# Kernel optimization log

Measured on AMD Instinct MI355X. Metric: run time of the kernel, lower is better.

## Reference

```python
import jax, jax.numpy as jnp
import numpy as np

K_MIN = 30.0
TAU = 1e-06
BETA = 0.9
LAMBDA_MAX = 0.1
LAMBDA_SCALE = 1.0

N, D_OUT, N_MODULES, N_CONTEXTS = 262144, 128, 64, 16


def setup_inputs() -> dict:
    key = jax.random.key(0)
    k1, k2, k3, k4 = jax.random.split(key, 4)
    Y_hat = jax.random.normal(k1, (N, D_OUT), dtype=jnp.float32)
    context_weights = jax.random.uniform(k2, (N, N_CONTEXTS), dtype=jnp.float32)
    M_pinv = jax.random.normal(k3, (N_MODULES, D_OUT), dtype=jnp.float32) * 0.1
    C_prior = jax.random.normal(k4, (N_CONTEXTS, N_MODULES, N_MODULES), dtype=jnp.float32) * 0.1
    # Buffers exactly as registered in __init__
    ema_Sigma = jnp.broadcast_to(jnp.eye(N_MODULES, dtype=jnp.float32), (N_CONTEXTS, N_MODULES, N_MODULES))
    ema_sigma_sq = jnp.ones((N_CONTEXTS, N_MODULES), dtype=jnp.float32)
    ema_initialized = jnp.zeros((N_CONTEXTS,), dtype=bool)
    return {"Y_hat": Y_hat, "context_weights": context_weights, "M_pinv": M_pinv,
            "C_prior": C_prior, "ema_Sigma": ema_Sigma, "ema_sigma_sq": ema_sigma_sq,
            "ema_initialized": ema_initialized}


def reference(Y_hat, context_weights, M_pinv, C_prior, ema_Sigma, ema_sigma_sq, ema_initialized):
    # Z_hat: [N, m]
    Z = Y_hat @ M_pinv.T
    wsum = context_weights.sum(axis=0)            # [T] == eff_n per context
    active = wsum >= K_MIN                        # context skipping, vectorized
    # Weighted mean per context: [T, m]
    mu = (context_weights.T @ Z) / wsum[:, None]
    # Weighted covariance: sum_n w_norm * (z-mu)(z-mu)^T == E_w[zz^T] - mu mu^T
    w_norm = context_weights / wsum[None, :]      # [N, T]
    S = jnp.einsum('nt,nm,nk->tmk', w_norm, Z, Z)  # [T, m, m]
    Sigma = S - mu[:, :, None] * mu[:, None, :]
    # EMA sigma_sq update (no-grad in original -> stop_gradient)
    Sigma_sg = jax.lax.stop_gradient(Sigma)
    diag_init = jnp.diagonal(Sigma_sg, axis1=1, axis2=2)                       # first-call branch
    diag_ema = jnp.diagonal(BETA * ema_Sigma + (1.0 - BETA) * Sigma_sg, axis1=1, axis2=2)
    sigma_sq = jnp.where(ema_initialized[:, None], diag_ema, diag_init)        # [T, m]
    std = jnp.sqrt(sigma_sq + TAU)
    denom = std[:, :, None] * std[:, None, :]
    C_hat = jnp.clip(Sigma / (denom + TAU), -1.0, 1.0)
    loss_t = jnp.sum((C_hat - C_prior) ** 2, axis=(1, 2)) / wsum               # [T]
    n_active = jnp.sum(active)
    total = jnp.sum(jnp.where(active, loss_t, 0.0))
    total = jnp.where(n_active > 0,
                      LAMBDA_MAX * LAMBDA_SCALE * total / jnp.maximum(n_active, 1).astype(total.dtype),
                      jnp.zeros((), total.dtype))
    return total
```

## Files before the change

### kernel.cpp

```cpp
#include <hip/hip_runtime.h>
#include <stdint.h>

#define N_ROWS 262144
#define D_OUTC 128
#define M_MOD  64
#define T_CTX  16

#define ZB_OFF   ((size_t)0)
#define ZB_BYTES ((size_t)M_MOD * N_ROWS * 2)
#define WT_OFF   (ZB_OFF + ZB_BYTES)
#define WT_BYTES ((size_t)T_CTX * N_ROWS * 2)
#define SS_OFF   (WT_OFF + WT_BYTES)
#define SS_BYTES ((size_t)T_CTX * M_MOD * M_MOD * 4)
#define B_OFF    (SS_OFF + SS_BYTES)
#define B_BYTES  ((size_t)T_CTX * M_MOD * 4)
#define WSUM_OFF (B_OFF + B_BYTES)
#define WSUM_BYTES ((size_t)64)
#define LT_OFF   (WSUM_OFF + WSUM_BYTES)
#define LT_BYTES ((size_t)64)
#define PSS_OFF  (LT_OFF + LT_BYTES)
#define PSS_BYTES ((size_t)256 * T_CTX * M_MOD * M_MOD * 2)
#define NEED_BIG (PSS_OFF + PSS_BYTES)

typedef __attribute__((ext_vector_type(4))) float f32x4;
typedef __attribute__((ext_vector_type(8))) _Float16 f16x8;
typedef __attribute__((ext_vector_type(2))) _Float16 h2;

union FR { uint4 u; f16x8 v; h2 h[4]; };

__device__ __forceinline__ float bf2f(unsigned short u) {
  return __uint_as_float(((unsigned int)u) << 16);
}
__device__ __forceinline__ unsigned short f2bf(float f) {
  unsigned int x = __float_as_uint(f);
  return (unsigned short)((x + 0x7fffu + ((x >> 16) & 1u)) >> 16);
}
__device__ __forceinline__ h2 cvt_pkrtz(float a, float b) {
  return __builtin_bit_cast(h2, __builtin_amdgcn_cvt_pkrtz(a, b));
}
#if __has_builtin(__builtin_amdgcn_fdot2)
__device__ __forceinline__ float fdot2f(h2 a, h2 b, float c) {
  return __builtin_amdgcn_fdot2(a, b, c, false);
}
#else
__device__ __forceinline__ float fdot2f(h2 a, h2 b, float c) {
  return c + (float)a[0] * (float)b[0] + (float)a[1] * (float)b[1];
}
#endif

#define WAITVM(N) asm volatile("s_waitcnt vmcnt(" #N ")" ::: "memory")
#define SBAR() do { __builtin_amdgcn_s_barrier(); __builtin_amdgcn_sched_barrier(0); } while (0)

__global__ __launch_bounds__(256) void wtr_kernel(const float* __restrict__ W,
                                                  _Float16* __restrict__ Wt)
{
  __shared__ float Wf[16][260];
  const int tid = threadIdx.x;
  const int n0  = blockIdx.x * 256;
  {
    const float4* src = (const float4*)(W + (size_t)(n0 + tid) * T_CTX);
#pragma unroll
    for (int q = 0; q < 4; ++q) {
      float4 v = src[q];
      Wf[q * 4 + 0][tid] = v.x; Wf[q * 4 + 1][tid] = v.y;
      Wf[q * 4 + 2][tid] = v.z; Wf[q * 4 + 3][tid] = v.w;
    }
  }
  __syncthreads();
  const int t = tid >> 4, c0 = (tid & 15) * 16;
  FR o[2];
#pragma unroll
  for (int j = 0; j < 2; ++j)
#pragma unroll
    for (int p = 0; p < 4; ++p)
      o[j].h[p] = cvt_pkrtz(Wf[t][c0 + j * 8 + 2 * p], Wf[t][c0 + j * 8 + 2 * p + 1]);
  uint4* dst = (uint4*)(Wt + (size_t)t * N_ROWS + n0 + c0);
  dst[0] = o[0].u; dst[1] = o[1].u;
}

__global__ __launch_bounds__(256, 6) void zk_kernel(
    const float* __restrict__ Y, const float* __restrict__ Mp,
    _Float16* __restrict__ Zbt)
{
  __shared__ __align__(16) _Float16 Mpl[64 * 128];
  const int tid = threadIdx.x;
  const int l   = tid & 63;
  const int wv  = tid >> 6;
  const int g   = l >> 4;
  const int col = l & 15;
  {
    const int m  = tid >> 2;
    const int dq = tid & 3;
#pragma unroll
    for (int i = 0; i < 4; ++i) {
      const int s = dq * 4 + i;
      const float* mp = Mp + (size_t)m * D_OUTC + s * 8;
      float4 a = *(const float4*)mp;
      float4 b = *(const float4*)(mp + 4);
      FR o;
      o.h[0] = cvt_pkrtz(a.x, a.y); o.h[1] = cvt_pkrtz(a.z, a.w);
      o.h[2] = cvt_pkrtz(b.x, b.y); o.h[3] = cvt_pkrtz(b.z, b.w);
      const int ss = (s & ~7) | ((s & 7) ^ (m & 7));
      *(uint4*)((char*)&Mpl[0] + m * 256 + ss * 16) = o.u;
    }
  }
  __syncthreads();
#pragma unroll
  for (int it = 0; it < 2; ++it) {
    const int n0 = (blockIdx.x * 2 + it) * 64;
    const int nr = n0 + wv * 16 + col;
    const float* __restrict__ yr = Y + (size_t)nr * D_OUTC;
    float4 yv[8];
#pragma unroll
    for (int ks = 0; ks < 4; ++ks) {
      yv[2 * ks]     = *(const float4*)(yr + ks * 32 + g * 8);
      yv[2 * ks + 1] = *(const float4*)(yr + ks * 32 + g * 8 + 4);
    }
    f32x4 acc[4];
#pragma unroll
    for (int qi = 0; qi < 4; ++qi) acc[qi] = (f32x4){0.f, 0.f, 0.f, 0.f};
#pragma unroll
    for (int ks = 0; ks < 4; ++ks) {
      const float* f0 = (const float*)&yv[2 * ks];
      const float* f1 = (const float*)&yv[2 * ks + 1];
      FR B;
      B.h[0] = cvt_pkrtz(f0[0], f0[1]); B.h[1] = cvt_pkrtz(f0[2], f0[3]);
      B.h[2] = cvt_pkrtz(f1[0], f1[1]); B.h[3] = cvt_pkrtz(f1[2], f1[3]);
#pragma unroll
      for (int qi = 0; qi < 4; ++qi) {
        const int m = qi * 16 + col;
        const int s = ks * 4 + g;
        FR A;
        A.u = *(const uint4*)((char*)&Mpl[0] + m * 256 + 16 * ((s & ~7) | ((s & 7) ^ (m & 7))));
        acc[qi] = __builtin_amdgcn_mfma_f32_16x16x32_f16(A.v, B.v, acc[qi], 0, 0, 0);
      }
    }
#pragma unroll
    for (int qi = 0; qi < 4; ++qi)
#pragma unroll
      for (int i = 0; i < 4; ++i)
        Zbt[(size_t)(qi * 16 + g * 4 + i) * N_ROWS + n0 + wv * 16 + col] =
            (_Float16)acc[qi][i];
  }
}

#define SS_NS 256
#define NCH   16
template <bool PARTIAL>
__global__ __launch_bounds__(512, 4) void ss_kernel(
    const _Float16* __restrict__ Zbt, const _Float16* __restrict__ Wt,
    float* __restrict__ SS, float* __restrict__ Bm,
    unsigned short* __restrict__ Pss)
{
  __shared__ __align__(16) _Float16 Zl[4][64 * 64];
  __shared__ __align__(16) _Float16 Wlds[8 * 1024];
  const int tid = threadIdx.x;
  const int l   = tid & 63;
  const int wv  = tid >> 6;
  const int g   = l >> 4;
  const int col = l & 15;
  const int ns  = blockIdx.x & (SS_NS - 1);
  const int cg  = blockIdx.x >> 8;
  const int ctx = cg * 8 + wv;
  const int n0b = ns * 1024;

  f32x4 acc[4][4];
  f32x4 accB[4];
#pragma unroll
  for (int a = 0; a < 4; ++a) {
    accB[a] = (f32x4){0.f, 0.f, 0.f, 0.f};
#pragma unroll
    for (int b = 0; b < 4; ++b) acc[a][b] = (f32x4){0.f, 0.f, 0.f, 0.f};
  }
  FR ones;
#pragma unroll
  for (int j = 0; j < 4; ++j) ones.h[j] = (h2){(_Float16)1.f, (_Float16)1.f};

#pragma unroll
  for (int k = 0; k < 2; ++k) {
    const _Float16* wsrc = Wt + (size_t)ctx * N_ROWS + n0b + k * 512 + l * 8;
    __builtin_amdgcn_global_load_lds((const unsigned int*)wsrc,
        (unsigned int*)((char*)&Wlds[0] + wv * 2048 + k * 1024), 16, 0, 0);
  }
  const int zrow  = 8 * wv + (l >> 3);
  const int zslot = l & 7;
  auto stage = [&](int c) {
    const int n0 = n0b + c * 64;
    const _Float16* src = Zbt + (size_t)zrow * N_ROWS + n0 + 8 * (zslot ^ (zrow & 7));
    __builtin_amdgcn_global_load_lds((const unsigned int*)src,
        (unsigned int*)((char*)&Zl[c & 3][0] + wv * 1024 + l * 16), 16, 0, 0);
  };

  stage(0); stage(1); stage(2);
  WAITVM(2);
  SBAR();

  for (int c = 0; c < NCH; ++c) {
    if (c + 3 < NCH) stage(c + 3);
    const char* zb = (const char*)&Zl[c & 3][0];
    const char* wb = (const char*)&Wlds[0] + wv * 2048 + c * 128;
#pragma unroll
    for (int s = 0; s < 2; ++s) {
      FR wfr;
      wfr.u = *(const uint4*)(wb + s * 64 + g * 16);
      FR fr[4];
#pragma unroll
      for (int qi = 0; qi < 4; ++qi) {
        const int r = qi * 16 + col;
        fr[qi].u = *(const uint4*)(zb + r * 128 + 16 * ((s * 4 + g) ^ (r & 7)));
      }
      __builtin_amdgcn_s_setprio(1);
#pragma unroll
      for (int qi = 0; qi < 4; ++qi) {
        FR A;
#pragma unroll
        for (int j = 0; j < 4; ++j) A.h[j] = fr[qi].h[j] * wfr.h[j];
        accB[qi] = __builtin_amdgcn_mfma_f32_16x16x32_f16(A.v, ones.v, accB[qi], 0, 0, 0);
#pragma unroll
        for (int ki = 0; ki < 4; ++ki)
          acc[qi][ki] = __builtin_amdgcn_mfma_f32_16x16x32_f16(A.v, fr[ki].v, acc[qi][ki], 0, 0, 0);
      }
      __builtin_amdgcn_s_setprio(0);
    }
    if (c + 3 < NCH)       { WAITVM(2); SBAR(); }
    else if (c == NCH - 3) { WAITVM(1); SBAR(); }
    else if (c == NCH - 2) { WAITVM(0); SBAR(); }
  }

  if (col == 0) {
#pragma unroll
    for (int qi = 0; qi < 4; ++qi)
#pragma unroll
      for (int i = 0; i < 4; ++i)
        atomicAdd(&Bm[ctx * 64 + qi * 16 + g * 4 + i], accB[qi][i]);
  }
  if (PARTIAL) {
    unsigned short* P = Pss + ((size_t)ns * 16 + ctx) * 4096;
#pragma unroll
    for (int qi = 0; qi < 4; ++qi)
#pragma unroll
      for (int ki = 0; ki < 4; ++ki)
#pragma unroll
        for (int i = 0; i < 4; ++i)
          P[(qi * 16 + g * 4 + i) * 64 + ki * 16 + col] = f2bf(acc[qi][ki][i]);
  } else {
#pragma unroll
    for (int qi = 0; qi < 4; ++qi)
#pragma unroll
      for (int ki = 0; ki < 4; ++ki)
#pragma unroll
        for (int i = 0; i < 4; ++i)
          atomicAdd(&SS[(size_t)ctx * 4096 + (qi * 16 + g * 4 + i) * 64 + ki * 16 + col],
                    acc[qi][ki][i]);
  }
}

__global__ __launch_bounds__(256) void wsk_kernel(const _Float16* __restrict__ Wt,
                                                  float* __restrict__ wsum)
{
  const int tid = threadIdx.x;
  const int t = blockIdx.x >> 2, q = blockIdx.x & 3;
  const uint4* base = (const uint4*)(Wt + (size_t)t * N_ROWS + q * 65536);
  const h2 one2 = {(_Float16)1.f, (_Float16)1.f};
  float s = 0.f;
  for (int i = tid; i < 8192; i += 256) {
    uint4 v = base[i];
    const h2* h = (const h2*)&v;
#pragma unroll
    for (int j = 0; j < 4; ++j) s = fdot2f(h[j], one2, s);
  }
  s += __shfl_xor(s, 1);  s += __shfl_xor(s, 2);
  s += __shfl_xor(s, 4);  s += __shfl_xor(s, 8);
  s += __shfl_xor(s, 16); s += __shfl_xor(s, 32);
  __shared__ float red[4];
  if ((tid & 63) == 0) red[tid >> 6] = s;
  __syncthreads();
  if (tid == 0) atomicAdd(&wsum[t], red[0] + red[1] + red[2] + red[3]);
}

__global__ __launch_bounds__(256) void ssred_kernel(
    const unsigned short* __restrict__ Pss, float* __restrict__ SS)
{
  const int e = blockIdx.x * 256 + threadIdx.x;
  float s = 0.f;
#pragma unroll 8
  for (int b = 0; b < 256; ++b)
    s += bf2f(Pss[(size_t)b * 65536 + e]);
  SS[e] = s;
}

__global__ __launch_bounds__(64) void fin1_kernel(
    const float* __restrict__ SS, const float* __restrict__ Bm,
    const float* __restrict__ wsum, const float* __restrict__ Cp,
    const float* __restrict__ emaS, const unsigned char* __restrict__ inited,
    float* __restrict__ LT)
{
  const int t = blockIdx.x, m = threadIdx.x;
  __shared__ float muL[64], stdL[64];
  const float ws  = wsum[t];
  const float inv = 1.0f / ws;
  const float mu  = Bm[t * 64 + m] * inv;
  {
    float Smm = SS[(size_t)t * 4096 + m * 65] * inv - mu * mu;
    float de  = 0.9f * emaS[(size_t)t * 4096 + m * 65] + 0.1f * Smm;
    float sq  = inited[t] ? de : Smm;
    muL[m]  = mu;
    stdL[m] = sqrtf(sq + 1e-6f);
  }
  __syncthreads();
  const float sm = stdL[m];
  const float* SSr = SS + (size_t)t * 4096 + m * 64;
  const float* Cpr = Cp + (size_t)t * 4096 + m * 64;
  float acc = 0.f;
#pragma unroll
  for (int k = 0; k < 64; ++k) {
    float Sig = SSr[k] * inv - mu * muL[k];
    float den = sm * stdL[k] + 1e-6f;
    float ch  = fminf(1.f, fmaxf(-1.f, Sig / den));
    float d   = ch - Cpr[k];
    acc = fmaf(d, d, acc);
  }
#pragma unroll
  for (int o = 1; o < 64; o <<= 1) acc += __shfl_xor(acc, o);
  if (m == 0) LT[t] = acc * inv;
}

__global__ __launch_bounds__(64) void fin2_kernel(
    const float* __restrict__ LT, const float* __restrict__ wsum,
    float* __restrict__ out)
{
  const int l = threadIdx.x;
  float lt = 0.f, act = 0.f;
  if (l < 16) {
    float ws = wsum[l];
    if (ws >= 30.0f) { act = 1.f; lt = LT[l]; }
  }
#pragma unroll
  for (int o = 1; o < 16; o <<= 1) {
    lt  += __shfl_xor(lt, o);
    act += __shfl_xor(act, o);
  }
  if (l == 0) out[0] = (act > 0.f) ? (0.1f * 1.0f * lt / act) : 0.f;
}

extern "C" void kernel_launch(void* const* d_in, const int* in_sizes, int n_in,
                              void* d_out, int out_size, void* d_ws, size_t ws_size,
                              hipStream_t stream) {
  (void)in_sizes; (void)n_in; (void)out_size;
  const float* Y    = (const float*)d_in[0];
  const float* W    = (const float*)d_in[1];
  const float* Mp   = (const float*)d_in[2];
  const float* Cp   = (const float*)d_in[3];
  const float* emaS = (const float*)d_in[4];
  const unsigned char* inited = (const unsigned char*)d_in[6];
  float* out = (float*)d_out;
  char* ws = (char*)d_ws;
  _Float16* Zbt = (_Float16*)(ws + ZB_OFF);
  _Float16* Wt  = (_Float16*)(ws + WT_OFF);
  float* SS   = (float*)(ws + SS_OFF);
  float* Bm   = (float*)(ws + B_OFF);
  float* wsum = (float*)(ws + WSUM_OFF);
  float* LT   = (float*)(ws + LT_OFF);
  unsigned short* Pss = (unsigned short*)(ws + PSS_OFF);

  wtr_kernel<<<N_ROWS / 256, 256, 0, stream>>>(W, Wt);
  zk_kernel<<<N_ROWS / 128, 256, 0, stream>>>(Y, Mp, Zbt);
  if (ws_size >= NEED_BIG) {
    (void)hipMemsetAsync(ws + B_OFF, 0, B_BYTES + WSUM_BYTES, stream);
    ss_kernel<true><<<2 * SS_NS, 512, 0, stream>>>(Zbt, Wt, SS, Bm, Pss);
    wsk_kernel<<<64, 256, 0, stream>>>(Wt, wsum);
    ssred_kernel<<<256, 256, 0, stream>>>(Pss, SS);
  } else {
    (void)hipMemsetAsync(ws + SS_OFF, 0, SS_BYTES + B_BYTES + WSUM_BYTES, stream);
    ss_kernel<false><<<2 * SS_NS, 512, 0, stream>>>(Zbt, Wt, SS, Bm, Pss);
    wsk_kernel<<<64, 256, 0, stream>>>(Wt, wsum);
  }
  fin1_kernel<<<16, 64, 0, stream>>>(SS, Bm, wsum, Cp, emaS, inited, LT);
  fin2_kernel<<<1, 64, 0, stream>>>(LT, wsum, out);
}
```

Before: 139.7 us.

## Fuse Z projection into covariance kernel and fold weight sums into transpose

Z = Y·M_pinv^T is now computed per 64-row chunk inside a single 1024-thread covariance kernel. Each chunk goes straight to shared memory, double-buffered with async Y loads, so the fp16 Z buffer is no longer written to and re-read from global memory. All 16 contexts are handled in one block, so each Z tile is shared by every context. Per-context weight sums are accumulated with atomics inside the transpose kernel, which removes the separate reduction kernel. The cost is a much larger shared-memory footprint per block and only 256 blocks with one block per CU, which may limit occupancy and latency hiding.

```diff
diff --git a/kernel.cpp b/kernel.cpp
--- a/kernel.cpp
+++ b/kernel.cpp
@@ -6,9 +6,7 @@
 #define M_MOD  64
 #define T_CTX  16
 
-#define ZB_OFF   ((size_t)0)
-#define ZB_BYTES ((size_t)M_MOD * N_ROWS * 2)
-#define WT_OFF   (ZB_OFF + ZB_BYTES)
+#define WT_OFF   ((size_t)0)
 #define WT_BYTES ((size_t)T_CTX * N_ROWS * 2)
 #define SS_OFF   (WT_OFF + WT_BYTES)
 #define SS_BYTES ((size_t)T_CTX * M_MOD * M_MOD * 4)
@@ -38,21 +36,14 @@
 __device__ __forceinline__ h2 cvt_pkrtz(float a, float b) {
   return __builtin_bit_cast(h2, __builtin_amdgcn_cvt_pkrtz(a, b));
 }
-#if __has_builtin(__builtin_amdgcn_fdot2)
-__device__ __forceinline__ float fdot2f(h2 a, h2 b, float c) {
-  return __builtin_amdgcn_fdot2(a, b, c, false);
-}
-#else
-__device__ __forceinline__ float fdot2f(h2 a, h2 b, float c) {
-  return c + (float)a[0] * (float)b[0] + (float)a[1] * (float)b[1];
-}
-#endif
 
 #define WAITVM(N) asm volatile("s_waitcnt vmcnt(" #N ")" ::: "memory")
+#define WAITLG()  asm volatile("s_waitcnt lgkmcnt(0)" ::: "memory")
 #define SBAR() do { __builtin_amdgcn_s_barrier(); __builtin_amdgcn_sched_barrier(0); } while (0)
 
 __global__ __launch_bounds__(256) void wtr_kernel(const float* __restrict__ W,
-                                                  _Float16* __restrict__ Wt)
+                                                  _Float16* __restrict__ Wt,
+                                                  float* __restrict__ wsum)
 {
   __shared__ float Wf[16][260];
   const int tid = threadIdx.x;
@@ -69,136 +60,122 @@
   __syncthreads();
   const int t = tid >> 4, c0 = (tid & 15) * 16;
   FR o[2];
+  float s = 0.f;
 #pragma unroll
   for (int j = 0; j < 2; ++j)
 #pragma unroll
-    for (int p = 0; p < 4; ++p)
-      o[j].h[p] = cvt_pkrtz(Wf[t][c0 + j * 8 + 2 * p], Wf[t][c0 + j * 8 + 2 * p + 1]);
+    for (int p = 0; p < 4; ++p) {
+      float a = Wf[t][c0 + j * 8 + 2 * p], b = Wf[t][c0 + j * 8 + 2 * p + 1];
+      o[j].h[p] = cvt_pkrtz(a, b);
+      s += a + b;
+    }
   uint4* dst = (uint4*)(Wt + (size_t)t * N_ROWS + n0 + c0);
   dst[0] = o[0].u; dst[1] = o[1].u;
-}
-
-__global__ __launch_bounds__(256, 6) void zk_kernel(
+  s += __shfl_xor(s, 1); s += __shfl_xor(s, 2);
+  s += __shfl_xor(s, 4); s += __shfl_xor(s, 8);
+  if ((tid & 15) == 0) atomicAdd(&wsum[t], s);
+}
+
+#define NCH 16
+template <bool PARTIAL>
+__global__ __launch_bounds__(1024, 4) void fuse_kernel(
     const float* __restrict__ Y, const float* __restrict__ Mp,
-    _Float16* __restrict__ Zbt)
-{
+    const _Float16* __restrict__ Wt,
+    float* __restrict__ SS, float* __restrict__ Bm,
+    unsigned short* __restrict__ Pss)
+{
+  __shared__ __align__(16) float    Yl[2][64 * 128];
+  __shared__ __align__(16) _Float16 Zl[2][64 * 64];
   __shared__ __align__(16) _Float16 Mpl[64 * 128];
+  __shared__ __align__(16) _Float16 Wlds[16 * 1024];
   const int tid = threadIdx.x;
   const int l   = tid & 63;
   const int wv  = tid >> 6;
   const int g   = l >> 4;
   const int col = l & 15;
+  const int ns  = blockIdx.x;
+  const int n0b = ns * 1024;
+  const int mq  = wv & 3, nq = wv >> 2;
+
+  f32x4 acc[4][4];
+  f32x4 accB[4];
+#pragma unroll
+  for (int a = 0; a < 4; ++a) {
+    accB[a] = (f32x4){0.f, 0.f, 0.f, 0.f};
+#pragma unroll
+    for (int b = 0; b < 4; ++b) acc[a][b] = (f32x4){0.f, 0.f, 0.f, 0.f};
+  }
+  FR ones;
+#pragma unroll
+  for (int j = 0; j < 4; ++j) ones.h[j] = (h2){(_Float16)1.f, (_Float16)1.f};
+
   {
-    const int m  = tid >> 2;
-    const int dq = tid & 3;
-#pragma unroll
-    for (int i = 0; i < 4; ++i) {
-      const int s = dq * 4 + i;
-      const float* mp = Mp + (size_t)m * D_OUTC + s * 8;
-      float4 a = *(const float4*)mp;
-      float4 b = *(const float4*)(mp + 4);
-      FR o;
-      o.h[0] = cvt_pkrtz(a.x, a.y); o.h[1] = cvt_pkrtz(a.z, a.w);
-      o.h[2] = cvt_pkrtz(b.x, b.y); o.h[3] = cvt_pkrtz(b.z, b.w);
-      const int ss = (s & ~7) | ((s & 7) ^ (m & 7));
-      *(uint4*)((char*)&Mpl[0] + m * 256 + ss * 16) = o.u;
-    }
-  }
-  __syncthreads();
-#pragma unroll
-  for (int it = 0; it < 2; ++it) {
-    const int n0 = (blockIdx.x * 2 + it) * 64;
-    const int nr = n0 + wv * 16 + col;
-    const float* __restrict__ yr = Y + (size_t)nr * D_OUTC;
-    float4 yv[8];
+    const int m = tid >> 4;
+    const int s = tid & 15;
+    const float* mp = Mp + (size_t)m * D_OUTC + s * 8;
+    float4 a = *(const float4*)mp;
+    float4 b = *(const float4*)(mp + 4);
+    FR o;
+    o.h[0] = cvt_pkrtz(a.x, a.y); o.h[1] = cvt_pkrtz(a.z, a.w);
+    o.h[2] = cvt_pkrtz(b.x, b.y); o.h[3] = cvt_pkrtz(b.z, b.w);
+    const int ss2 = (s & ~7) | ((s & 7) ^ (m & 7));
+    *(uint4*)((char*)Mpl + m * 256 + ss2 * 16) = o.u;
+  }
+#pragma unroll
+  for (int j = 0; j < 2; ++j) {
+    const int o = j * 16384 + tid * 16;
+    const int t = o >> 11;
+    const int noff = (o & 2047) >> 1;
+    const _Float16* src = Wt + (size_t)t * N_ROWS + n0b + noff;
+    __builtin_amdgcn_global_load_lds((const unsigned int*)src,
+        (unsigned int*)((char*)Wlds + o), 16, 0, 0);
+  }
+  auto stageY = [&](int c) {
+    const int nb = n0b + c * 64;
+#pragma unroll
+    for (int j = 0; j < 2; ++j) {
+      const int o = j * 16384 + tid * 16;
+      const int r = o >> 9;
+      const int qp = (o >> 4) & 31;
+      const int q = (qp & ~7) | ((qp & 7) ^ (r & 7));
+      const float* src = Y + (size_t)(nb + r) * D_OUTC + q * 4;
+      __builtin_amdgcn_global_load_lds((const unsigned int*)src,
+          (unsigned int*)((char*)&Yl[c & 1][0] + o), 16, 0, 0);
+    }
+  };
+  auto produce = [&](int c) {
+    const char* yb = (const char*)&Yl[c & 1][0];
+    const int rB = nq * 16 + col;
+    f32x4 pacc = (f32x4){0.f, 0.f, 0.f, 0.f};
 #pragma unroll
     for (int ks = 0; ks < 4; ++ks) {
-      yv[2 * ks]     = *(const float4*)(yr + ks * 32 + g * 8);
-      yv[2 * ks + 1] = *(const float4*)(yr + ks * 32 + g * 8 + 4);
-    }
-    f32x4 acc[4];
-#pragma unroll
-    for (int qi = 0; qi < 4; ++qi) acc[qi] = (f32x4){0.f, 0.f, 0.f, 0.f};
-#pragma unroll
-    for (int ks = 0; ks < 4; ++ks) {
-      const float* f0 = (const float*)&yv[2 * ks];
-      const float* f1 = (const float*)&yv[2 * ks + 1];
+      const int q0 = ks * 8 + 2 * g;
+      const int q1 = q0 + 1;
+      uint4 y0 = *(const uint4*)(yb + rB * 512 + 16 * ((q0 & ~7) | ((q0 & 7) ^ (rB & 7))));
+      uint4 y1 = *(const uint4*)(yb + rB * 512 + 16 * ((q1 & ~7) | ((q1 & 7) ^ (rB & 7))));
+      const float* f0 = (const float*)&y0;
+      const float* f1 = (const float*)&y1;
       FR B;
       B.h[0] = cvt_pkrtz(f0[0], f0[1]); B.h[1] = cvt_pkrtz(f0[2], f0[3]);
       B.h[2] = cvt_pkrtz(f1[0], f1[1]); B.h[3] = cvt_pkrtz(f1[2], f1[3]);
-#pragma unroll
-      for (int qi = 0; qi < 4; ++qi) {
-        const int m = qi * 16 + col;
-        const int s = ks * 4 + g;
-        FR A;
-        A.u = *(const uint4*)((char*)&Mpl[0] + m * 256 + 16 * ((s & ~7) | ((s & 7) ^ (m & 7))));
-        acc[qi] = __builtin_amdgcn_mfma_f32_16x16x32_f16(A.v, B.v, acc[qi], 0, 0, 0);
-      }
-    }
-#pragma unroll
-    for (int qi = 0; qi < 4; ++qi)
-#pragma unroll
-      for (int i = 0; i < 4; ++i)
-        Zbt[(size_t)(qi * 16 + g * 4 + i) * N_ROWS + n0 + wv * 16 + col] =
-            (_Float16)acc[qi][i];
-  }
-}
-
-#define SS_NS 256
-#define NCH   16
-template <bool PARTIAL>
-__global__ __launch_bounds__(512, 4) void ss_kernel(
-    const _Float16* __restrict__ Zbt, const _Float16* __restrict__ Wt,
-    float* __restrict__ SS, float* __restrict__ Bm,
-    unsigned short* __restrict__ Pss)
-{
-  __shared__ __align__(16) _Float16 Zl[4][64 * 64];
-  __shared__ __align__(16) _Float16 Wlds[8 * 1024];
-  const int tid = threadIdx.x;
-  const int l   = tid & 63;
-  const int wv  = tid >> 6;
-  const int g   = l >> 4;
-  const int col = l & 15;
-  const int ns  = blockIdx.x & (SS_NS - 1);
-  const int cg  = blockIdx.x >> 8;
-  const int ctx = cg * 8 + wv;
-  const int n0b = ns * 1024;
-
-  f32x4 acc[4][4];
-  f32x4 accB[4];
-#pragma unroll
-  for (int a = 0; a < 4; ++a) {
-    accB[a] = (f32x4){0.f, 0.f, 0.f, 0.f};
-#pragma unroll
-    for (int b = 0; b < 4; ++b) acc[a][b] = (f32x4){0.f, 0.f, 0.f, 0.f};
-  }
-  FR ones;
-#pragma unroll
-  for (int j = 0; j < 4; ++j) ones.h[j] = (h2){(_Float16)1.f, (_Float16)1.f};
-
-#pragma unroll
-  for (int k = 0; k < 2; ++k) {
-    const _Float16* wsrc = Wt + (size_t)ctx * N_ROWS + n0b + k * 512 + l * 8;
-    __builtin_amdgcn_global_load_lds((const unsigned int*)wsrc,
-        (unsigned int*)((char*)&Wlds[0] + wv * 2048 + k * 1024), 16, 0, 0);
-  }
-  const int zrow  = 8 * wv + (l >> 3);
-  const int zslot = l & 7;
-  auto stage = [&](int c) {
-    const int n0 = n0b + c * 64;
-    const _Float16* src = Zbt + (size_t)zrow * N_ROWS + n0 + 8 * (zslot ^ (zrow & 7));
-    __builtin_amdgcn_global_load_lds((const unsigned int*)src,
-        (unsigned int*)((char*)&Zl[c & 3][0] + wv * 1024 + l * 16), 16, 0, 0);
+      const int mA = mq * 16 + col;
+      const int s2 = ks * 4 + g;
+      FR A;
+      A.u = *(const uint4*)((char*)Mpl + mA * 256 + 16 * ((s2 & ~7) | ((s2 & 7) ^ (mA & 7))));
+      pacc = __builtin_amdgcn_mfma_f32_16x16x32_f16(A.v, B.v, pacc, 0, 0, 0);
+    }
+    char* zb = (char*)&Zl[c & 1][0];
+#pragma unroll
+    for (int i = 0; i < 4; ++i) {
+      const int rm = mq * 16 + g * 4 + i;
+      const int sn = nq * 2 + (col >> 3);
+      const int by = rm * 128 + 16 * (sn ^ (rm & 7)) + (col & 7) * 2;
+      *(_Float16*)(zb + by) = (_Float16)pacc[i];
+    }
   };
-
-  stage(0); stage(1); stage(2);
-  WAITVM(2);
-  SBAR();
-
-  for (int c = 0; c < NCH; ++c) {
-    if (c + 3 < NCH) stage(c + 3);
-    const char* zb = (const char*)&Zl[c & 3][0];
-    const char* wb = (const char*)&Wlds[0] + wv * 2048 + c * 128;
+  auto consume = [&](int c) {
+    const char* zb = (const char*)&Zl[c & 1][0];
+    const char* wb = (const char*)Wlds + wv * 2048 + c * 128;
 #pragma unroll
     for (int s = 0; s < 2; ++s) {
       FR wfr;
@@ -222,20 +199,34 @@
       }
       __builtin_amdgcn_s_setprio(0);
     }
-    if (c + 3 < NCH)       { WAITVM(2); SBAR(); }
-    else if (c == NCH - 3) { WAITVM(1); SBAR(); }
-    else if (c == NCH - 2) { WAITVM(0); SBAR(); }
-  }
+  };
+
+  stageY(0);
+  stageY(1);
+  WAITLG();
+  WAITVM(2);
+  SBAR();
+
+  for (int c = 0; c < NCH - 2; ++c) {
+    if (c) WAITVM(2);
+    produce(c);
+    WAITLG();
+    SBAR();
+    stageY(c + 2);
+    consume(c);
+  }
+  WAITVM(2); produce(14); WAITLG(); SBAR(); consume(14);
+  WAITVM(0); produce(15); WAITLG(); SBAR(); consume(15);
 
   if (col == 0) {
 #pragma unroll
     for (int qi = 0; qi < 4; ++qi)
 #pragma unroll
       for (int i = 0; i < 4; ++i)
-        atomicAdd(&Bm[ctx * 64 + qi * 16 + g * 4 + i], accB[qi][i]);
+        atomicAdd(&Bm[wv * 64 + qi * 16 + g * 4 + i], accB[qi][i]);
   }
   if (PARTIAL) {
-    unsigned short* P = Pss + ((size_t)ns * 16 + ctx) * 4096;
+    unsigned short* P = Pss + ((size_t)ns * 16 + wv) * 4096;
 #pragma unroll
     for (int qi = 0; qi < 4; ++qi)
 #pragma unroll
@@ -250,32 +241,9 @@
       for (int ki = 0; ki < 4; ++ki)
 #pragma unroll
         for (int i = 0; i < 4; ++i)
-          atomicAdd(&SS[(size_t)ctx * 4096 + (qi * 16 + g * 4 + i) * 64 + ki * 16 + col],
+          atomicAdd(&SS[(size_t)wv * 4096 + (qi * 16 + g * 4 + i) * 64 + ki * 16 + col],
                     acc[qi][ki][i]);
   }
-}
-
-__global__ __launch_bounds__(256) void wsk_kernel(const _Float16* __restrict__ Wt,
-                                                  float* __restrict__ wsum)
-{
-  const int tid = threadIdx.x;
-  const int t = blockIdx.x >> 2, q = blockIdx.x & 3;
-  const uint4* base = (const uint4*)(Wt + (size_t)t * N_ROWS + q * 65536);
-  const h2 one2 = {(_Float16)1.f, (_Float16)1.f};
-  float s = 0.f;
-  for (int i = tid; i < 8192; i += 256) {
-    uint4 v = base[i];
-    const h2* h = (const h2*)&v;
-#pragma unroll
-    for (int j = 0; j < 4; ++j) s = fdot2f(h[j], one2, s);
-  }
-  s += __shfl_xor(s, 1);  s += __shfl_xor(s, 2);
-  s += __shfl_xor(s, 4);  s += __shfl_xor(s, 8);
-  s += __shfl_xor(s, 16); s += __shfl_xor(s, 32);
-  __shared__ float red[4];
-  if ((tid & 63) == 0) red[tid >> 6] = s;
-  __syncthreads();
-  if (tid == 0) atomicAdd(&wsum[t], red[0] + red[1] + red[2] + red[3]);
 }
 
 __global__ __launch_bounds__(256) void ssred_kernel(
@@ -355,7 +323,6 @@
   const unsigned char* inited = (const unsigned char*)d_in[6];
   float* out = (float*)d_out;
   char* ws = (char*)d_ws;
-  _Float16* Zbt = (_Float16*)(ws + ZB_OFF);
   _Float16* Wt  = (_Float16*)(ws + WT_OFF);
   float* SS   = (float*)(ws + SS_OFF);
   float* Bm   = (float*)(ws + B_OFF);
@@ -363,17 +330,15 @@
   float* LT   = (float*)(ws + LT_OFF);
   unsigned short* Pss = (unsigned short*)(ws + PSS_OFF);
 
-  wtr_kernel<<<N_ROWS / 256, 256, 0, stream>>>(W, Wt);
-  zk_kernel<<<N_ROWS / 128, 256, 0, stream>>>(Y, Mp, Zbt);
   if (ws_size >= NEED_BIG) {
     (void)hipMemsetAsync(ws + B_OFF, 0, B_BYTES + WSUM_BYTES, stream);
-    ss_kernel<true><<<2 * SS_NS, 512, 0, stream>>>(Zbt, Wt, SS, Bm, Pss);
-    wsk_kernel<<<64, 256, 0, stream>>>(Wt, wsum);
+    wtr_kernel<<<N_ROWS / 256, 256, 0, stream>>>(W, Wt, wsum);
+    fuse_kernel<true><<<256, 1024, 0, stream>>>(Y, Mp, Wt, SS, Bm, Pss);
     ssred_kernel<<<256, 256, 0, stream>>>(Pss, SS);
   } else {
     (void)hipMemsetAsync(ws + SS_OFF, 0, SS_BYTES + B_BYTES + WSUM_BYTES, stream);
-    ss_kernel<false><<<2 * SS_NS, 512, 0, stream>>>(Zbt, Wt, SS, Bm, Pss);
-    wsk_kernel<<<64, 256, 0, stream>>>(Wt, wsum);
+    wtr_kernel<<<N_ROWS / 256, 256, 0, stream>>>(W, Wt, wsum);
+    fuse_kernel<false><<<256, 1024, 0, stream>>>(Y, Mp, Wt, SS, Bm, Pss);
   }
   fin1_kernel<<<16, 64, 0, stream>>>(SS, Bm, wsum, Cp, emaS, inited, LT);
   fin2_kernel<<<1, 64, 0, stream>>>(LT, wsum, out);
```

Result: slower. 195.9 us (+40.3%).

## Fuse W transpose and wsum into Z kernel, fold partial reduction into finalizer

Applied to the files above, without the earlier changes.

Merges the W transpose and per-context weight-sum reduction into the Z projection kernel, with atomic wsum accumulation on padded slots. It also folds the bf16 partial-sum reduction into a 1024-thread fin1 kernel, and vectorizes the Z stores by swapping MFMA operand order. The ss_kernel block index is remapped so both context groups of one slice run adjacently. This removes three launches and a re-read of Wt, at the cost of more atomics and a reduction handled by only 16 blocks.

```diff
diff --git a/kernel.cpp b/kernel.cpp
--- a/kernel.cpp
+++ b/kernel.cpp
@@ -15,7 +15,7 @@
 #define B_OFF    (SS_OFF + SS_BYTES)
 #define B_BYTES  ((size_t)T_CTX * M_MOD * 4)
 #define WSUM_OFF (B_OFF + B_BYTES)
-#define WSUM_BYTES ((size_t)64)
+#define WSUM_BYTES ((size_t)1024)
 #define LT_OFF   (WSUM_OFF + WSUM_BYTES)
 #define LT_BYTES ((size_t)64)
 #define PSS_OFF  (LT_OFF + LT_BYTES)
@@ -38,56 +38,25 @@
 __device__ __forceinline__ h2 cvt_pkrtz(float a, float b) {
   return __builtin_bit_cast(h2, __builtin_amdgcn_cvt_pkrtz(a, b));
 }
-#if __has_builtin(__builtin_amdgcn_fdot2)
-__device__ __forceinline__ float fdot2f(h2 a, h2 b, float c) {
-  return __builtin_amdgcn_fdot2(a, b, c, false);
-}
-#else
-__device__ __forceinline__ float fdot2f(h2 a, h2 b, float c) {
-  return c + (float)a[0] * (float)b[0] + (float)a[1] * (float)b[1];
-}
-#endif
 
 #define WAITVM(N) asm volatile("s_waitcnt vmcnt(" #N ")" ::: "memory")
 #define SBAR() do { __builtin_amdgcn_s_barrier(); __builtin_amdgcn_sched_barrier(0); } while (0)
 
-__global__ __launch_bounds__(256) void wtr_kernel(const float* __restrict__ W,
-                                                  _Float16* __restrict__ Wt)
-{
-  __shared__ float Wf[16][260];
-  const int tid = threadIdx.x;
-  const int n0  = blockIdx.x * 256;
-  {
-    const float4* src = (const float4*)(W + (size_t)(n0 + tid) * T_CTX);
-#pragma unroll
-    for (int q = 0; q < 4; ++q) {
-      float4 v = src[q];
-      Wf[q * 4 + 0][tid] = v.x; Wf[q * 4 + 1][tid] = v.y;
-      Wf[q * 4 + 2][tid] = v.z; Wf[q * 4 + 3][tid] = v.w;
-    }
-  }
-  __syncthreads();
-  const int t = tid >> 4, c0 = (tid & 15) * 16;
-  FR o[2];
-#pragma unroll
-  for (int j = 0; j < 2; ++j)
-#pragma unroll
-    for (int p = 0; p < 4; ++p)
-      o[j].h[p] = cvt_pkrtz(Wf[t][c0 + j * 8 + 2 * p], Wf[t][c0 + j * 8 + 2 * p + 1]);
-  uint4* dst = (uint4*)(Wt + (size_t)t * N_ROWS + n0 + c0);
-  dst[0] = o[0].u; dst[1] = o[1].u;
-}
-
-__global__ __launch_bounds__(256, 6) void zk_kernel(
+__global__ __launch_bounds__(256, 4) void zkw_kernel(
     const float* __restrict__ Y, const float* __restrict__ Mp,
-    _Float16* __restrict__ Zbt)
+    const float* __restrict__ W,
+    _Float16* __restrict__ Zbt, _Float16* __restrict__ Wt,
+    float* __restrict__ wsum)
 {
   __shared__ __align__(16) _Float16 Mpl[64 * 128];
+  __shared__ float Wf[16][132];
   const int tid = threadIdx.x;
   const int l   = tid & 63;
   const int wv  = tid >> 6;
   const int g   = l >> 4;
   const int col = l & 15;
+  const int n0  = blockIdx.x * 128;
+
   {
     const int m  = tid >> 2;
     const int dq = tid & 3;
@@ -100,16 +69,38 @@
       FR o;
       o.h[0] = cvt_pkrtz(a.x, a.y); o.h[1] = cvt_pkrtz(a.z, a.w);
       o.h[2] = cvt_pkrtz(b.x, b.y); o.h[3] = cvt_pkrtz(b.z, b.w);
-      const int ss = (s & ~7) | ((s & 7) ^ (m & 7));
-      *(uint4*)((char*)&Mpl[0] + m * 256 + ss * 16) = o.u;
-    }
+      const int ss2 = (s & ~7) | ((s & 7) ^ (m & 7));
+      *(uint4*)((char*)Mpl + m * 256 + ss2 * 16) = o.u;
+    }
+  }
+  {
+    const int r  = tid >> 1;
+    const int hh = (tid & 1) * 8;
+    const float* wr = W + (size_t)(n0 + r) * T_CTX + hh;
+    float4 a = *(const float4*)wr;
+    float4 b = *(const float4*)(wr + 4);
+    Wf[hh + 0][r] = a.x; Wf[hh + 1][r] = a.y; Wf[hh + 2][r] = a.z; Wf[hh + 3][r] = a.w;
+    Wf[hh + 4][r] = b.x; Wf[hh + 5][r] = b.y; Wf[hh + 6][r] = b.z; Wf[hh + 7][r] = b.w;
   }
   __syncthreads();
+  {
+    const int t = tid >> 4, seg = tid & 15;
+    float v[8];
+#pragma unroll
+    for (int p = 0; p < 8; ++p) v[p] = Wf[t][seg * 8 + p];
+    FR o;
+#pragma unroll
+    for (int p = 0; p < 4; ++p) o.h[p] = cvt_pkrtz(v[2 * p], v[2 * p + 1]);
+    *(uint4*)(Wt + (size_t)t * N_ROWS + n0 + seg * 8) = o.u;
+    float s = ((v[0] + v[1]) + (v[2] + v[3])) + ((v[4] + v[5]) + (v[6] + v[7]));
+    s += __shfl_xor(s, 1); s += __shfl_xor(s, 2);
+    s += __shfl_xor(s, 4); s += __shfl_xor(s, 8);
+    if ((l & 15) == 0) atomicAdd(&wsum[t * 16], s);
+  }
 #pragma unroll
   for (int it = 0; it < 2; ++it) {
-    const int n0 = (blockIdx.x * 2 + it) * 64;
-    const int nr = n0 + wv * 16 + col;
-    const float* __restrict__ yr = Y + (size_t)nr * D_OUTC;
+    const int nt = n0 + it * 64 + wv * 16;
+    const float* __restrict__ yr = Y + (size_t)(nt + col) * D_OUTC;
     float4 yv[8];
 #pragma unroll
     for (int ks = 0; ks < 4; ++ks) {
@@ -123,29 +114,31 @@
     for (int ks = 0; ks < 4; ++ks) {
       const float* f0 = (const float*)&yv[2 * ks];
       const float* f1 = (const float*)&yv[2 * ks + 1];
-      FR B;
-      B.h[0] = cvt_pkrtz(f0[0], f0[1]); B.h[1] = cvt_pkrtz(f0[2], f0[3]);
-      B.h[2] = cvt_pkrtz(f1[0], f1[1]); B.h[3] = cvt_pkrtz(f1[2], f1[3]);
+      FR Yf;
+      Yf.h[0] = cvt_pkrtz(f0[0], f0[1]); Yf.h[1] = cvt_pkrtz(f0[2], f0[3]);
+      Yf.h[2] = cvt_pkrtz(f1[0], f1[1]); Yf.h[3] = cvt_pkrtz(f1[2], f1[3]);
 #pragma unroll
       for (int qi = 0; qi < 4; ++qi) {
         const int m = qi * 16 + col;
         const int s = ks * 4 + g;
-        FR A;
-        A.u = *(const uint4*)((char*)&Mpl[0] + m * 256 + 16 * ((s & ~7) | ((s & 7) ^ (m & 7))));
-        acc[qi] = __builtin_amdgcn_mfma_f32_16x16x32_f16(A.v, B.v, acc[qi], 0, 0, 0);
+        FR Mf;
+        Mf.u = *(const uint4*)((char*)Mpl + m * 256 + 16 * ((s & ~7) | ((s & 7) ^ (m & 7))));
+        acc[qi] = __builtin_amdgcn_mfma_f32_16x16x32_f16(Yf.v, Mf.v, acc[qi], 0, 0, 0);
       }
     }
 #pragma unroll
-    for (int qi = 0; qi < 4; ++qi)
-#pragma unroll
-      for (int i = 0; i < 4; ++i)
-        Zbt[(size_t)(qi * 16 + g * 4 + i) * N_ROWS + n0 + wv * 16 + col] =
-            (_Float16)acc[qi][i];
-  }
-}
-
-#define SS_NS 256
-#define NCH   16
+    for (int qi = 0; qi < 4; ++qi) {
+      const int m = qi * 16 + col;
+      h2 lo, hi;
+      lo[0] = (_Float16)acc[qi][0]; lo[1] = (_Float16)acc[qi][1];
+      hi[0] = (_Float16)acc[qi][2]; hi[1] = (_Float16)acc[qi][3];
+      uint2 pk = {__builtin_bit_cast(unsigned int, lo), __builtin_bit_cast(unsigned int, hi)};
+      *(uint2*)(Zbt + (size_t)m * N_ROWS + nt + g * 4) = pk;
+    }
+  }
+}
+
+#define NCH 16
 template <bool PARTIAL>
 __global__ __launch_bounds__(512, 4) void ss_kernel(
     const _Float16* __restrict__ Zbt, const _Float16* __restrict__ Wt,
@@ -159,8 +152,9 @@
   const int wv  = tid >> 6;
   const int g   = l >> 4;
   const int col = l & 15;
-  const int ns  = blockIdx.x & (SS_NS - 1);
-  const int cg  = blockIdx.x >> 8;
+  const int x   = blockIdx.x;
+  const int cg  = (x >> 3) & 1;
+  const int ns  = (x & 7) | ((x >> 4) << 3);
   const int ctx = cg * 8 + wv;
   const int n0b = ns * 1024;
 
@@ -180,7 +174,7 @@
   for (int k = 0; k < 2; ++k) {
     const _Float16* wsrc = Wt + (size_t)ctx * N_ROWS + n0b + k * 512 + l * 8;
     __builtin_amdgcn_global_load_lds((const unsigned int*)wsrc,
-        (unsigned int*)((char*)&Wlds[0] + wv * 2048 + k * 1024), 16, 0, 0);
+        (unsigned int*)((char*)Wlds + wv * 2048 + k * 1024), 16, 0, 0);
   }
   const int zrow  = 8 * wv + (l >> 3);
   const int zslot = l & 7;
@@ -198,7 +192,7 @@
   for (int c = 0; c < NCH; ++c) {
     if (c + 3 < NCH) stage(c + 3);
     const char* zb = (const char*)&Zl[c & 3][0];
-    const char* wb = (const char*)&Wlds[0] + wv * 2048 + c * 128;
+    const char* wb = (const char*)Wlds + wv * 2048 + c * 128;
 #pragma unroll
     for (int s = 0; s < 2; ++s) {
       FR wfr;
@@ -255,74 +249,71 @@
   }
 }
 
-__global__ __launch_bounds__(256) void wsk_kernel(const _Float16* __restrict__ Wt,
-                                                  float* __restrict__ wsum)
+template <bool PARTIAL>
+__global__ __launch_bounds__(1024) void fin1_kernel(
+    const unsigned short* __restrict__ Pss, const float* __restrict__ SSg,
+    const float* __restrict__ Bm, const float* __restrict__ wsum,
+    const float* __restrict__ Cp, const float* __restrict__ emaS,
+    const unsigned char* __restrict__ inited, float* __restrict__ LT)
 {
-  const int tid = threadIdx.x;
-  const int t = blockIdx.x >> 2, q = blockIdx.x & 3;
-  const uint4* base = (const uint4*)(Wt + (size_t)t * N_ROWS + q * 65536);
-  const h2 one2 = {(_Float16)1.f, (_Float16)1.f};
-  float s = 0.f;
-  for (int i = tid; i < 8192; i += 256) {
-    uint4 v = base[i];
-    const h2* h = (const h2*)&v;
-#pragma unroll
-    for (int j = 0; j < 4; ++j) s = fdot2f(h[j], one2, s);
-  }
-  s += __shfl_xor(s, 1);  s += __shfl_xor(s, 2);
-  s += __shfl_xor(s, 4);  s += __shfl_xor(s, 8);
-  s += __shfl_xor(s, 16); s += __shfl_xor(s, 32);
-  __shared__ float red[4];
-  if ((tid & 63) == 0) red[tid >> 6] = s;
+  __shared__ float SSl[4096];
+  __shared__ float muL[64], stdL[64];
+  __shared__ float red[16];
+  const int t = blockIdx.x, tid = threadIdx.x;
+  if (PARTIAL) {
+    float s0 = 0.f, s1 = 0.f, s2 = 0.f, s3 = 0.f;
+    const unsigned short* P = Pss + (size_t)t * 4096 + tid * 4;
+#pragma unroll 4
+    for (int b = 0; b < 256; ++b) {
+      uint2 v = *(const uint2*)(P + (size_t)b * 65536);
+      s0 += bf2f((unsigned short)(v.x & 0xffffu));
+      s1 += bf2f((unsigned short)(v.x >> 16));
+      s2 += bf2f((unsigned short)(v.y & 0xffffu));
+      s3 += bf2f((unsigned short)(v.y >> 16));
+    }
+    SSl[tid * 4 + 0] = s0; SSl[tid * 4 + 1] = s1;
+    SSl[tid * 4 + 2] = s2; SSl[tid * 4 + 3] = s3;
+  } else {
+    float4 v = *(const float4*)(SSg + (size_t)t * 4096 + tid * 4);
+    *(float4*)&SSl[tid * 4] = v;
+  }
   __syncthreads();
-  if (tid == 0) atomicAdd(&wsum[t], red[0] + red[1] + red[2] + red[3]);
-}
-
-__global__ __launch_bounds__(256) void ssred_kernel(
-    const unsigned short* __restrict__ Pss, float* __restrict__ SS)
-{
-  const int e = blockIdx.x * 256 + threadIdx.x;
-  float s = 0.f;
-#pragma unroll 8
-  for (int b = 0; b < 256; ++b)
-    s += bf2f(Pss[(size_t)b * 65536 + e]);
-  SS[e] = s;
-}
-
-__global__ __launch_bounds__(64) void fin1_kernel(
-    const float* __restrict__ SS, const float* __restrict__ Bm,
-    const float* __restrict__ wsum, const float* __restrict__ Cp,
-    const float* __restrict__ emaS, const unsigned char* __restrict__ inited,
-    float* __restrict__ LT)
-{
-  const int t = blockIdx.x, m = threadIdx.x;
-  __shared__ float muL[64], stdL[64];
-  const float ws  = wsum[t];
+  const float ws  = wsum[t * 16];
   const float inv = 1.0f / ws;
-  const float mu  = Bm[t * 64 + m] * inv;
-  {
-    float Smm = SS[(size_t)t * 4096 + m * 65] * inv - mu * mu;
+  if (tid < 64) {
+    const int m = tid;
+    float mu  = Bm[t * 64 + m] * inv;
+    float Smm = SSl[m * 65] * inv - mu * mu;
     float de  = 0.9f * emaS[(size_t)t * 4096 + m * 65] + 0.1f * Smm;
     float sq  = inited[t] ? de : Smm;
     muL[m]  = mu;
     stdL[m] = sqrtf(sq + 1e-6f);
   }
   __syncthreads();
-  const float sm = stdL[m];
-  const float* SSr = SS + (size_t)t * 4096 + m * 64;
-  const float* Cpr = Cp + (size_t)t * 4096 + m * 64;
+  const int m  = tid >> 4;
+  const int k0 = (tid & 15) * 4;
+  float4 cp4 = *(const float4*)(Cp + (size_t)t * 4096 + tid * 4);
+  const float* cpp = (const float*)&cp4;
   float acc = 0.f;
 #pragma unroll
-  for (int k = 0; k < 64; ++k) {
-    float Sig = SSr[k] * inv - mu * muL[k];
-    float den = sm * stdL[k] + 1e-6f;
+  for (int j = 0; j < 4; ++j) {
+    const int k = k0 + j;
+    float Sig = SSl[m * 64 + k] * inv - muL[m] * muL[k];
+    float den = stdL[m] * stdL[k] + 1e-6f;
     float ch  = fminf(1.f, fmaxf(-1.f, Sig / den));
-    float d   = ch - Cpr[k];
+    float d   = ch - cpp[j];
     acc = fmaf(d, d, acc);
   }
 #pragma unroll
   for (int o = 1; o < 64; o <<= 1) acc += __shfl_xor(acc, o);
-  if (m == 0) LT[t] = acc * inv;
+  if ((tid & 63) == 0) red[tid >> 6] = acc;
+  __syncthreads();
+  if (tid == 0) {
+    float s = 0.f;
+#pragma unroll
+    for (int i = 0; i < 16; ++i) s += red[i];
+    LT[t] = s * inv;
+  }
 }
 
 __global__ __launch_bounds__(64) void fin2_kernel(
@@ -332,7 +323,7 @@
   const int l = threadIdx.x;
   float lt = 0.f, act = 0.f;
   if (l < 16) {
-    float ws = wsum[l];
+    float ws = wsum[l * 16];
     if (ws >= 30.0f) { act = 1.f; lt = LT[l]; }
   }
 #pragma unroll
@@ -363,18 +354,16 @@
   float* LT   = (float*)(ws + LT_OFF);
   unsigned short* Pss = (unsigned short*)(ws + PSS_OFF);
 
-  wtr_kernel<<<N_ROWS / 256, 256, 0, stream>>>(W, Wt);
-  zk_kernel<<<N_ROWS / 128, 256, 0, stream>>>(Y, Mp, Zbt);
   if (ws_size >= NEED_BIG) {
     (void)hipMemsetAsync(ws + B_OFF, 0, B_BYTES + WSUM_BYTES, stream);
-    ss_kernel<true><<<2 * SS_NS, 512, 0, stream>>>(Zbt, Wt, SS, Bm, Pss);
-    wsk_kernel<<<64, 256, 0, stream>>>(Wt, wsum);
-    ssred_kernel<<<256, 256, 0, stream>>>(Pss, SS);
+    zkw_kernel<<<N_ROWS / 128, 256, 0, stream>>>(Y, Mp, W, Zbt, Wt, wsum);
+    ss_kernel<true><<<512, 512, 0, stream>>>(Zbt, Wt, SS, Bm, Pss);
+    fin1_kernel<true><<<16, 1024, 0, stream>>>(Pss, SS, Bm, wsum, Cp, emaS, inited, LT);
   } else {
     (void)hipMemsetAsync(ws + SS_OFF, 0, SS_BYTES + B_BYTES + WSUM_BYTES, stream);
-    ss_kernel<false><<<2 * SS_NS, 512, 0, stream>>>(Zbt, Wt, SS, Bm, Pss);
-    wsk_kernel<<<64, 256, 0, stream>>>(Wt, wsum);
-  }
-  fin1_kernel<<<16, 64, 0, stream>>>(SS, Bm, wsum, Cp, emaS, inited, LT);
+    zkw_kernel<<<N_ROWS / 128, 256, 0, stream>>>(Y, Mp, W, Zbt, Wt, wsum);
+    ss_kernel<false><<<512, 512, 0, stream>>>(Zbt, Wt, SS, Bm, Pss);
+    fin1_kernel<false><<<16, 1024, 0, stream>>>(Pss, SS, Bm, wsum, Cp, emaS, inited, LT);
+  }
   fin2_kernel<<<1, 64, 0, stream>>>(LT, wsum, out);
 }
```

Measured after the change: 152.6 us. 1.09x slower.

## Stage Y tiles into LDS with double-buffered async loads in Z projection kernel

Applied to the files above, without the earlier changes.

The Z = Y·M_pinv^T kernel now streams Y through a double-buffered, swizzled LDS tile using global_load_lds instead of per-thread register loads. Each block handles 256 rows in 8 chunks, with the loads for the next chunk overlapping the MFMA work on the current one. The work split also changes so each wave covers 16 rows by 32 modules. This is meant to hide global-load latency and improve memory throughput for the 128 MB Y read, at the cost of more LDS per block, lower occupancy (launch bounds 6 to 3) and half as many blocks.

```diff
diff --git a/kernel.cpp b/kernel.cpp
--- a/kernel.cpp
+++ b/kernel.cpp
@@ -78,16 +78,20 @@
   dst[0] = o[0].u; dst[1] = o[1].u;
 }
 
-__global__ __launch_bounds__(256, 6) void zk_kernel(
+#define ZCH 8
+__global__ __launch_bounds__(256, 3) void zk_kernel(
     const float* __restrict__ Y, const float* __restrict__ Mp,
     _Float16* __restrict__ Zbt)
 {
+  __shared__ __align__(16) float    Yl[2][32 * 128];
   __shared__ __align__(16) _Float16 Mpl[64 * 128];
-  const int tid = threadIdx.x;
-  const int l   = tid & 63;
-  const int wv  = tid >> 6;
-  const int g   = l >> 4;
-  const int col = l & 15;
+  const int tid  = threadIdx.x;
+  const int l    = tid & 63;
+  const int wv   = tid >> 6;
+  const int g    = l >> 4;
+  const int col  = l & 15;
+  const int n0b  = blockIdx.x * 256;
+
   {
     const int m  = tid >> 2;
     const int dq = tid & 3;
@@ -104,31 +108,45 @@
       *(uint4*)((char*)&Mpl[0] + m * 256 + ss * 16) = o.u;
     }
   }
+  auto stage = [&](int c) {
+#pragma unroll
+    for (int k = 0; k < 4; ++k) {
+      const int pr  = wv * 4 + k;
+      const int row = pr * 2 + (l >> 5);
+      const int q   = l & 31;
+      const int b   = (q & ~7) | ((q & 7) ^ (row & 7));
+      const float* src = Y + ((size_t)(n0b + c * 32 + row)) * D_OUTC + b * 4;
+      __builtin_amdgcn_global_load_lds((const unsigned int*)src,
+          (unsigned int*)((char*)&Yl[c & 1][0] + pr * 1024), 16, 0, 0);
+    }
+  };
+
+  stage(0);
   __syncthreads();
-#pragma unroll
-  for (int it = 0; it < 2; ++it) {
-    const int n0 = (blockIdx.x * 2 + it) * 64;
-    const int nr = n0 + wv * 16 + col;
-    const float* __restrict__ yr = Y + (size_t)nr * D_OUTC;
-    float4 yv[8];
+
+  const int ntile = wv & 1;
+  const int mh    = wv >> 1;
+  const int nrow  = ntile * 16 + col;
+
+  for (int c = 0; c < ZCH; ++c) {
+    if (c + 1 < ZCH) stage(c + 1);
+    const char* ybase = (const char*)&Yl[c & 1][0];
+    f32x4 acc[2];
+    acc[0] = (f32x4){0.f, 0.f, 0.f, 0.f};
+    acc[1] = (f32x4){0.f, 0.f, 0.f, 0.f};
 #pragma unroll
     for (int ks = 0; ks < 4; ++ks) {
-      yv[2 * ks]     = *(const float4*)(yr + ks * 32 + g * 8);
-      yv[2 * ks + 1] = *(const float4*)(yr + ks * 32 + g * 8 + 4);
-    }
-    f32x4 acc[4];
-#pragma unroll
-    for (int qi = 0; qi < 4; ++qi) acc[qi] = (f32x4){0.f, 0.f, 0.f, 0.f};
-#pragma unroll
-    for (int ks = 0; ks < 4; ++ks) {
-      const float* f0 = (const float*)&yv[2 * ks];
-      const float* f1 = (const float*)&yv[2 * ks + 1];
+      const char* yb = ybase + nrow * 512 + ks * 128;
+      uint4 y0 = *(const uint4*)(yb + 16 * ((2 * g) ^ (nrow & 7)));
+      uint4 y1 = *(const uint4*)(yb + 16 * ((2 * g + 1) ^ (nrow & 7)));
+      const float* f0 = (const float*)&y0;
+      const float* f1 = (const float*)&y1;
       FR B;
       B.h[0] = cvt_pkrtz(f0[0], f0[1]); B.h[1] = cvt_pkrtz(f0[2], f0[3]);
       B.h[2] = cvt_pkrtz(f1[0], f1[1]); B.h[3] = cvt_pkrtz(f1[2], f1[3]);
 #pragma unroll
-      for (int qi = 0; qi < 4; ++qi) {
-        const int m = qi * 16 + col;
+      for (int qi = 0; qi < 2; ++qi) {
+        const int m = (mh * 2 + qi) * 16 + col;
         const int s = ks * 4 + g;
         FR A;
         A.u = *(const uint4*)((char*)&Mpl[0] + m * 256 + 16 * ((s & ~7) | ((s & 7) ^ (m & 7))));
@@ -136,11 +154,15 @@
       }
     }
 #pragma unroll
-    for (int qi = 0; qi < 4; ++qi)
+    for (int qi = 0; qi < 2; ++qi)
 #pragma unroll
       for (int i = 0; i < 4; ++i)
-        Zbt[(size_t)(qi * 16 + g * 4 + i) * N_ROWS + n0 + wv * 16 + col] =
+        Zbt[(size_t)((mh * 2 + qi) * 16 + g * 4 + i) * N_ROWS + n0b + c * 32 + ntile * 16 + col] =
             (_Float16)acc[qi][i];
+    if (c + 1 < ZCH) {
+      WAITVM(8);
+      SBAR();
+    }
   }
 }
 
@@ -180,7 +202,7 @@
   for (int k = 0; k < 2; ++k) {
     const _Float16* wsrc = Wt + (size_t)ctx * N_ROWS + n0b + k * 512 + l * 8;
     __builtin_amdgcn_global_load_lds((const unsigned int*)wsrc,
-        (unsigned int*)((char*)&Wlds[0] + wv * 2048 + k * 1024), 16, 0, 0);
+        (unsigned int*)((char*)Wlds + wv * 2048 + k * 1024), 16, 0, 0);
   }
   const int zrow  = 8 * wv + (l >> 3);
   const int zslot = l & 7;
@@ -198,7 +220,7 @@
   for (int c = 0; c < NCH; ++c) {
     if (c + 3 < NCH) stage(c + 3);
     const char* zb = (const char*)&Zl[c & 3][0];
-    const char* wb = (const char*)&Wlds[0] + wv * 2048 + c * 128;
+    const char* wb = (const char*)Wlds + wv * 2048 + c * 128;
 #pragma unroll
     for (int s = 0; s < 2; ++s) {
       FR wfr;
@@ -364,7 +386,7 @@
   unsigned short* Pss = (unsigned short*)(ws + PSS_OFF);
 
   wtr_kernel<<<N_ROWS / 256, 256, 0, stream>>>(W, Wt);
-  zk_kernel<<<N_ROWS / 128, 256, 0, stream>>>(Y, Mp, Zbt);
+  zk_kernel<<<N_ROWS / 256, 256, 0, stream>>>(Y, Mp, Zbt);
   if (ws_size >= NEED_BIG) {
     (void)hipMemsetAsync(ws + B_OFF, 0, B_BYTES + WSUM_BYTES, stream);
     ss_kernel<true><<<2 * SS_NS, 512, 0, stream>>>(Zbt, Wt, SS, Bm, Pss);
```

Measured after the change: 141.0 us. About the same (+1.0%).
